# Kernel optimization log

Hardware: AMD Instinct MI355X
Metric: run time of the kernel (lower is better)

The kernel has to match this reference:

```python
import jax, jax.numpy as jnp
import numpy as np

NEG_INF = -1e9


def setup_inputs() -> dict:
    key = jax.random.key(0)
    k1, k2, k3 = jax.random.split(key, 3)
    B, C, Q, D = 32, 2048, 128, 128
    context = jax.random.normal(k1, (B, C, D), dtype=jnp.float32)
    query = jax.random.normal(k2, (B, Q, D), dtype=jnp.float32)
    # Dense(1, use_bias=False) over concat([c, q, c*q]) -> weight vector of length 3*D
    w = jax.random.normal(k3, (3 * D,), dtype=jnp.float32) * (1.0 / np.sqrt(3 * D))
    query_mask = jnp.ones((B, Q), dtype=jnp.int32)
    return {"context": context, "query": query, "w": w, "query_mask": query_mask}


def reference(context, query, w, query_mask):
    # context: [B, C, D], query: [B, Q, D], w: [3D], query_mask: [B, Q]
    D = context.shape[-1]
    w1, w2, w3 = w[:D], w[D:2 * D], w[2 * D:]
    # Trilinear similarity, exactly equal to Dense(1)(concat([c_tiled, q_tiled, c*q]))
    # S[b,c,q] = context[b,c]·w1 + query[b,q]·w2 + (context[b,c]*w3)·query[b,q]
    S = (context @ w1)[:, :, None] \
        + (query @ w2)[:, None, :] \
        + jnp.einsum('bcd,bqd->bcq', context * w3, query)  # [B, C, Q]
    mask_add = (1.0 - query_mask.astype(jnp.float32))[:, None, :] * NEG_INF
    S = S + mask_add
    a = jax.nn.softmax(S, axis=2)                  # context-to-query attention [B, C, Q]
    c2q = jnp.einsum('bcq,bqd->bcd', a, query)     # [B, C, D]
    b = jax.nn.softmax(jnp.max(S, axis=2), axis=1) # query-to-context weights [B, C]
    q2c = jnp.einsum('bc,bcd->bd', b, context)[:, None, :]  # [B, 1, D]
    q2c = jnp.broadcast_to(q2c, context.shape)     # tile over c_len
    out = jnp.concatenate([context, c2q, context * c2q, context * q2c], axis=-1)
    return out  # [B, C, 4D]
```

## Files before the change

### kernel.cpp

```cpp
#include <hip/hip_runtime.h>
#include <cstdint>

#define B_ 32
#define C_ 2048
#define Q_ 128
#define D_ 128
#define CT 64
#define OFF_ 8.0f
#define NEG_INF_F (-1.0e9f)

typedef __attribute__((ext_vector_type(8))) short bf16x8;
typedef __attribute__((ext_vector_type(4))) float f32x4;

__device__ inline short bf16_rne(float v) {
    unsigned u = __float_as_uint(v);
    return (short)((u + 0x7FFFu + ((u >> 16) & 1u)) >> 16);
}
__device__ inline void split_f32(float v, short& h, short& l) {
    unsigned u  = __float_as_uint(v);
    unsigned hb = u & 0xffff0000u;
    float lo = v - __uint_as_float(hb);
    h = (short)(hb >> 16);
    l = (short)(__float_as_uint(lo) >> 16);
}

__global__ __launch_bounds__(256)
void cqa_prep(const float* __restrict__ qry, const float* __restrict__ w,
              const int* __restrict__ qmask, float* __restrict__ qw2e_g,
              unsigned short* __restrict__ qw3Hi, unsigned short* __restrict__ qTHi)
{
    const int b = blockIdx.y, ch = blockIdx.x;
    const int t = threadIdx.x;
    const float* qb = qry + (size_t)b * Q_ * D_;

    if (t < 32) {
        int rl = t >> 1, part = t & 1;
        int q = ch * 16 + rl;
        const float* p  = qb + q * D_ + part * 64;
        const float* wp = w + D_ + part * 64;
        float s = 0.f;
        #pragma unroll
        for (int j = 0; j < 64; j += 4) {
            float4 a4 = *(const float4*)(p + j);
            float4 w4 = *(const float4*)(wp + j);
            s += a4.x*w4.x + a4.y*w4.y + a4.z*w4.z + a4.w*w4.w;
        }
        s += __shfl_xor(s, 1, 2);
        if (!part) {
            float madd = (1.0f - (float)qmask[b * Q_ + q]) * NEG_INF_F;
            qw2e_g[b * Q_ + q] = s + madd;
        }
    }
    #pragma unroll
    for (int i = 0; i < 8; ++i) {
        int idx = t + i * 256;
        int ql = idx >> 7, d = idx & 127;
        int q = ch * 16 + ql;
        float v = qb[q * D_ + d];
        qw3Hi[((size_t)b * Q_ + q) * D_ + d] = (unsigned short)bf16_rne(v * w[2 * D_ + d]);
        qTHi[((size_t)b * D_ + d) * Q_ + q]  = (unsigned short)bf16_rne(v);
    }
}

__device__ __forceinline__ void stage_b(const unsigned short* __restrict__ gH,
                                        int col0, short* sb, int wv, int lane)
{
    #pragma unroll
    for (int j = 0; j < 2; ++j) {
        int seg = wv * 2 + j;
        int li  = seg * 64 + lane;
        int row = li >> 2;
        int col = (li & 3) * 8;
        __builtin_amdgcn_global_load_lds(
            (const __attribute__((address_space(1))) void*)(gH + (size_t)row * 128 + col0 + col),
            (__attribute__((address_space(3))) void*)(sb + seg * 512), 16, 0, 0);
    }
}

__global__ __launch_bounds__(256, 4)
void cqa_main(const float* __restrict__ ctx, const float* __restrict__ w,
              const float* __restrict__ qw2e_g,
              const unsigned short* __restrict__ qw3Hi, const unsigned short* __restrict__ qTHi,
              float* __restrict__ out, float* __restrict__ part, float* __restrict__ denp_g)
{
    __shared__ __align__(16) char smem[35840];
    short* SB   = (short*)smem;
    short* PHi  = (short*)(smem + 16384);
    float* Tr   = (float*)smem;
    float* red  = (float*)smem;
    float* mlds = (float*)(smem + 33792);
    float* dred = (float*)(smem + 34048);
    float* cw1  = (float*)(smem + 34304);
    float* qw2e = (float*)(smem + 34560);

    const int b   = blockIdx.y;
    const int c0  = blockIdx.x * CT;
    const int tid = threadIdx.x;
    const int lane = tid & 63;
    const int wv   = tid >> 6;
    const int w16  = wv * 16;
    const int lm   = lane & 15;
    const int lg   = lane >> 4;
    const int lk   = lg * 8;

    const float* ctxb = ctx + ((size_t)b * C_ + c0) * D_;
    const unsigned short* qw3Hb = qw3Hi + (size_t)b * Q_ * D_;
    const unsigned short* qTHb  = qTHi + (size_t)b * Q_ * D_;

    stage_b(qw3Hb, 0, SB, wv, lane);

    {
        int row = tid >> 2, part4 = tid & 3;
        const float* p  = ctxb + row * D_ + part4 * 32;
        const float* wp = w + part4 * 32;
        float s = 0.f;
        #pragma unroll
        for (int j = 0; j < 32; j += 4) {
            float4 c4 = *(const float4*)(p + j);
            float4 w4 = *(const float4*)(wp + j);
            s += c4.x*w4.x + c4.y*w4.y + c4.z*w4.z + c4.w*w4.w;
        }
        s += __shfl_xor(s, 1, 4);
        s += __shfl_xor(s, 2, 4);
        if (!part4) cw1[row] = s;
    }
    if (tid < Q_) qw2e[tid] = qw2e_g[b * Q_ + tid];

    const float* arow = ctxb + (size_t)(w16 + lm) * D_;
    bf16x8 aHr[4], aLr[4];
    #pragma unroll
    for (int t = 0; t < 4; ++t) {
        float4 v0 = *(const float4*)(arow + t * 32 + lk);
        float4 v1 = *(const float4*)(arow + t * 32 + lk + 4);
        float vv[8] = {v0.x, v0.y, v0.z, v0.w, v1.x, v1.y, v1.z, v1.w};
        #pragma unroll
        for (int i = 0; i < 8; ++i) {
            short hh, ll; split_f32(vv[i], hh, ll);
            aHr[t][i] = hh; aLr[t][i] = ll;
        }
    }
    __syncthreads();

    float qe[8];
    #pragma unroll
    for (int f = 0; f < 8; ++f) qe[f] = qw2e[f * 16 + lm];
    float cwr[4];
    #pragma unroll
    for (int r = 0; r < 4; ++r) cwr[r] = cw1[w16 + lg * 4 + r];

    const f32x4 vzero = {0.f, 0.f, 0.f, 0.f};
    f32x4 acc[8];
    #pragma unroll
    for (int f = 0; f < 8; ++f) acc[f] = vzero;

    #pragma unroll
    for (int t = 0; t < 4; ++t) {
        if (t < 3) stage_b(qw3Hb, (t + 1) * 32, SB + ((t + 1) & 1) * 4096, wv, lane);
        else       stage_b(qTHb,  0,            SB,                        wv, lane);
        const short* sb = SB + (t & 1) * 4096;
        bf16x8 aH = aHr[t], aL = aLr[t];
        #pragma unroll
        for (int f = 0; f < 8; ++f) {
            bf16x8 bH = *(const bf16x8*)(sb + (f * 16 + lm) * 32 + lk);
            acc[f] = __builtin_amdgcn_mfma_f32_16x16x32_bf16(aH, bH, acc[f], 0, 0, 0);
            acc[f] = __builtin_amdgcn_mfma_f32_16x16x32_bf16(aL, bH, acc[f], 0, 0, 0);
        }
        __syncthreads();
    }

    float inv[4];
    #pragma unroll
    for (int r = 0; r < 4; ++r) {
        float sv[8];
        float mx = -3.0e38f;
        #pragma unroll
        for (int f = 0; f < 8; ++f) {
            sv[f] = acc[f][r] + qe[f];
            mx = fmaxf(mx, sv[f]);
        }
        mx = fmaxf(mx, __shfl_xor(mx, 1, 16));
        mx = fmaxf(mx, __shfl_xor(mx, 2, 16));
        mx = fmaxf(mx, __shfl_xor(mx, 4, 16));
        mx = fmaxf(mx, __shfl_xor(mx, 8, 16));
        int lrow = w16 + lg * 4 + r;
        float s = 0.f;
        #pragma unroll
        for (int f = 0; f < 8; ++f) {
            float p = __expf(sv[f] - mx);
            s += p;
            PHi[lrow * 136 + f * 16 + lm] = bf16_rne(p);
        }
        s += __shfl_xor(s, 1, 16);
        s += __shfl_xor(s, 2, 16);
        s += __shfl_xor(s, 4, 16);
        s += __shfl_xor(s, 8, 16);
        inv[r] = 1.0f / s;
        if (lm == 0) mlds[lrow] = mx + cwr[r];
    }

    f32x4 acc2[8];
    #pragma unroll
    for (int f = 0; f < 8; ++f) acc2[f] = vzero;

    #pragma unroll
    for (int t = 0; t < 4; ++t) {
        if (t < 3) stage_b(qTHb, (t + 1) * 32, SB + ((t + 1) & 1) * 4096, wv, lane);
        const short* sb = SB + (t & 1) * 4096;
        bf16x8 aH = *(const bf16x8*)(PHi + (w16 + lm) * 136 + t * 32 + lk);
        #pragma unroll
        for (int f = 0; f < 8; ++f) {
            bf16x8 bH = *(const bf16x8*)(sb + (f * 16 + lm) * 32 + lk);
            acc2[f] = __builtin_amdgcn_mfma_f32_16x16x32_bf16(aH, bH, acc2[f], 0, 0, 0);
        }
        __syncthreads();
    }

    #pragma unroll
    for (int r = 0; r < 4; ++r) {
        int lrow = w16 + lg * 4 + r;
        #pragma unroll
        for (int f = 0; f < 8; ++f)
            Tr[lrow * 132 + f * 16 + lm] = acc2[f][r] * inv[r];
    }
    __syncthreads();

    const int rsel = tid >> 5;
    const int dd   = (tid & 31) * 4;
    float4 qacc = {0.f, 0.f, 0.f, 0.f};
    float denp = 0.f;
    #pragma unroll
    for (int pass = 0; pass < 8; ++pass) {
        int row = pass * 8 + rsel;
        float4 a  = *(const float4*)(Tr + row * 132 + dd);
        float4 cv = *(const float4*)(ctxb + (size_t)row * D_ + dd);
        float wgt = __expf(mlds[row] - OFF_);
        size_t obase = ((size_t)b * C_ + c0 + row) * (4 * D_);
        float4 p;
        p.x = cv.x*a.x; p.y = cv.y*a.y; p.z = cv.z*a.z; p.w = cv.w*a.w;
        *(float4*)(out + obase + dd)          = cv;
        *(float4*)(out + obase + D_ + dd)     = a;
        *(float4*)(out + obase + 2 * D_ + dd) = p;
        qacc.x += wgt * cv.x; qacc.y += wgt * cv.y;
        qacc.z += wgt * cv.z; qacc.w += wgt * cv.w;
        denp += wgt;
    }
    __syncthreads();
    *(float4*)(red + rsel * 128 + dd) = qacc;
    if ((tid & 31) == 0) dred[rsel] = denp;
    __syncthreads();
    if (tid < 128) {
        float s = 0.f;
        #pragma unroll
        for (int rr = 0; rr < 8; ++rr) s += red[rr * 128 + tid];
        part[((size_t)b * 32 + blockIdx.x) * 128 + tid] = s;
    }
    if (tid == 0) {
        float s = 0.f;
        #pragma unroll
        for (int rr = 0; rr < 8; ++rr) s += dred[rr];
        denp_g[b * 32 + blockIdx.x] = s;
    }
}

__global__ __launch_bounds__(128)
void cqa_q2c(const float* __restrict__ part, const float* __restrict__ denp_g,
             float* __restrict__ q2c)
{
    int b = blockIdx.x, d = threadIdx.x;
    float den = 0.f;
    #pragma unroll
    for (int j = 0; j < 32; ++j) den += denp_g[b * 32 + j];
    float s = 0.f;
    #pragma unroll
    for (int j = 0; j < 32; ++j) s += part[((size_t)b * 32 + j) * 128 + d];
    q2c[b * 128 + d] = s / den;
}

__global__ __launch_bounds__(256)
void cqa_out4(const float* __restrict__ ctx, const float* __restrict__ q2c,
              float* __restrict__ out)
{
    size_t i = (size_t)blockIdx.x * 256 + threadIdx.x;
    const size_t n4 = (size_t)B_*C_*D_/4;
    if (i >= n4) return;
    size_t bc = i >> 5;
    int d4 = (int)(i & 31);
    int b  = (int)(bc >> 11);
    float4 c4 = reinterpret_cast<const float4*>(ctx)[i];
    float4 g4 = reinterpret_cast<const float4*>(q2c)[b*32 + d4];
    float4 o;
    o.x = c4.x*g4.x; o.y = c4.y*g4.y; o.z = c4.z*g4.z; o.w = c4.w*g4.w;
    reinterpret_cast<float4*>(out)[bc*128 + 96 + d4] = o;
}

extern "C" void kernel_launch(void* const* d_in, const int* in_sizes, int n_in,
                              void* d_out, int out_size, void* d_ws, size_t ws_size,
                              hipStream_t stream)
{
    const float* ctx   = (const float*)d_in[0];
    const float* qry   = (const float*)d_in[1];
    const float* w     = (const float*)d_in[2];
    const int*   qmask = (const int*)d_in[3];
    float* out = (float*)d_out;
    float* ws  = (float*)d_ws;

    float* part    = ws;
    float* denp_g  = ws + 131072;
    float* q2c     = ws + 132096;
    float* qw2e_g  = ws + 136192;
    unsigned short* bf = (unsigned short*)(ws + 140288);
    unsigned short* qw3Hi = bf;
    unsigned short* qTHi  = bf + 524288;

    cqa_prep<<<dim3(8, B_), 256, 0, stream>>>(qry, w, qmask, qw2e_g, qw3Hi, qTHi);
    cqa_main<<<dim3(C_/CT, B_), 256, 0, stream>>>(ctx, w, qw2e_g, qw3Hi, qTHi,
                                                  out, part, denp_g);
    cqa_q2c<<<B_, 128, 0, stream>>>(part, denp_g, q2c);
    cqa_out4<<<(int)(((size_t)B_*C_*D_/4 + 255)/256), 256, 0, stream>>>(ctx, q2c, out);
}
```

Before: 57.99 us.

## Fuse q2c reduction and final output quarter into main kernel via cooperative grid sync

```diff
diff --git a/kernel.cpp b/kernel.cpp
--- a/kernel.cpp
+++ b/kernel.cpp
@@ -1,5 +1,8 @@
 #include <hip/hip_runtime.h>
+#include <hip/hip_cooperative_groups.h>
 #include <cstdint>
+
+namespace cg = cooperative_groups;
 
 #define B_ 32
 #define C_ 2048
@@ -77,6 +80,7 @@
     }
 }
 
+template<int COOP>
 __global__ __launch_bounds__(256, 4)
 void cqa_main(const float* __restrict__ ctx, const float* __restrict__ w,
               const float* __restrict__ qw2e_g,
@@ -226,6 +230,7 @@
 
     const int rsel = tid >> 5;
     const int dd   = (tid & 31) * 4;
+    float4 ctxs[8];
     float4 qacc = {0.f, 0.f, 0.f, 0.f};
     float denp = 0.f;
     #pragma unroll
@@ -233,6 +238,7 @@
         int row = pass * 8 + rsel;
         float4 a  = *(const float4*)(Tr + row * 132 + dd);
         float4 cv = *(const float4*)(ctxb + (size_t)row * D_ + dd);
+        ctxs[pass] = cv;
         float wgt = __expf(mlds[row] - OFF_);
         size_t obase = ((size_t)b * C_ + c0 + row) * (4 * D_);
         float4 p;
@@ -252,13 +258,50 @@
         float s = 0.f;
         #pragma unroll
         for (int rr = 0; rr < 8; ++rr) s += red[rr * 128 + tid];
-        part[((size_t)b * 32 + blockIdx.x) * 128 + tid] = s;
+        __hip_atomic_store(&part[((size_t)b * 32 + blockIdx.x) * 128 + tid], s,
+                           __ATOMIC_RELAXED, __HIP_MEMORY_SCOPE_AGENT);
     }
     if (tid == 0) {
         float s = 0.f;
         #pragma unroll
         for (int rr = 0; rr < 8; ++rr) s += dred[rr];
-        denp_g[b * 32 + blockIdx.x] = s;
+        __hip_atomic_store(&denp_g[b * 32 + blockIdx.x], s,
+                           __ATOMIC_RELAXED, __HIP_MEMORY_SCOPE_AGENT);
+    }
+
+    if constexpr (COOP) {
+        __threadfence();
+        cg::this_grid().sync();
+
+        float* q2c_lds = red;
+        float* dlds    = red + 128;
+        if (tid < 128) {
+            float s = 0.f;
+            #pragma unroll 8
+            for (int j = 0; j < 32; ++j)
+                s += __hip_atomic_load(&part[((size_t)b * 32 + j) * 128 + tid],
+                                       __ATOMIC_RELAXED, __HIP_MEMORY_SCOPE_AGENT);
+            q2c_lds[tid] = s;
+        } else if (tid < 160) {
+            dlds[tid - 128] = __hip_atomic_load(&denp_g[b * 32 + (tid - 128)],
+                                                __ATOMIC_RELAXED, __HIP_MEMORY_SCOPE_AGENT);
+        }
+        __syncthreads();
+        float den = 0.f;
+        #pragma unroll
+        for (int j = 0; j < 32; ++j) den += dlds[j];
+        float idn = 1.0f / den;
+        float4 qv = *(const float4*)(q2c_lds + dd);
+        qv.x *= idn; qv.y *= idn; qv.z *= idn; qv.w *= idn;
+        #pragma unroll
+        for (int pass = 0; pass < 8; ++pass) {
+            int row = pass * 8 + rsel;
+            float4 cv = ctxs[pass];
+            size_t obase = ((size_t)b * C_ + c0 + row) * (4 * D_);
+            float4 o;
+            o.x = cv.x*qv.x; o.y = cv.y*qv.y; o.z = cv.z*qv.z; o.w = cv.w*qv.w;
+            *(float4*)(out + obase + 3 * D_ + dd) = o;
+        }
     }
 }
 
@@ -313,8 +356,24 @@
     unsigned short* qTHi  = bf + 524288;
 
     cqa_prep<<<dim3(8, B_), 256, 0, stream>>>(qry, w, qmask, qw2e_g, qw3Hi, qTHi);
-    cqa_main<<<dim3(C_/CT, B_), 256, 0, stream>>>(ctx, w, qw2e_g, qw3Hi, qTHi,
-                                                  out, part, denp_g);
+
+    int dev = 0, cus = 0, maxb = 0;
+    hipGetDevice(&dev);
+    hipDeviceGetAttribute(&cus, hipDeviceAttributeMultiprocessorCount, dev);
+    hipOccupancyMaxActiveBlocksPerMultiprocessor(&maxb, (const void*)cqa_main<1>, 256, 0);
+
+    bool coop_ok = (cus > 0) && ((long)maxb * cus >= (long)(C_/CT) * B_);
+    if (coop_ok) {
+        void* args[] = { (void*)&ctx, (void*)&w, (void*)&qw2e_g,
+                         (void*)&qw3Hi, (void*)&qTHi,
+                         (void*)&out, (void*)&part, (void*)&denp_g };
+        hipError_t e = hipLaunchCooperativeKernel((const void*)cqa_main<1>,
+                                                  dim3(C_/CT, B_), dim3(256),
+                                                  args, 0, stream);
+        if (e == hipSuccess) return;
+    }
+    cqa_main<0><<<dim3(C_/CT, B_), 256, 0, stream>>>(ctx, w, qw2e_g, qw3Hi, qTHi,
+                                                     out, part, denp_g);
     cqa_q2c<<<B_, 128, 0, stream>>>(part, denp_g, q2c);
     cqa_out4<<<(int)(((size_t)B_*C_*D_/4 + 255)/256), 256, 0, stream>>>(ctx, q2c, out);
 }
```

Measured after the change: 57.89 us. About the same (-0.2%).
